# Kernel tuning notes

Measured on AMD Instinct MI355X. Metric: run time of the kernel, lower is better.

## Reference

```python
import jax, jax.numpy as jnp
import numpy as np

HEADS = 16  # init_kwargs['heads']


def setup_inputs() -> dict:
    key = jax.random.key(0)
    k1, k2, k3, k4, k5, k6 = jax.random.split(key, 6)
    N, L, E = 2, 2048, 1024
    return {
        "values": jax.random.normal(k1, (N, L, E), dtype=jnp.float32),
        "key": jax.random.normal(k2, (N, L, E), dtype=jnp.float32),
        "query": jax.random.normal(k3, (N, L, E), dtype=jnp.float32),
        "mask": jax.random.randint(k4, (N, 1, L, L), 0, 2, dtype=jnp.int32),
        # fc_out: Linear(heads*head_dim=E, E) with bias
        "W_out": jax.random.normal(k5, (E, E), dtype=jnp.float32) / np.sqrt(E),
        "b_out": jax.random.normal(k6, (E,), dtype=jnp.float32) * 0.01,
    }


def reference(values, key, query, mask, W_out, b_out):
    N, Lq, E = query.shape
    Lk = key.shape[1]
    H = HEADS
    D = E // H  # head_dim = 64
    q = query.reshape(N, Lq, H, D)
    k = key.reshape(N, Lk, H, D)
    v = values.reshape(N, Lk, H, D)
    # energy: (N, H, Q, K)
    energy = jnp.einsum("nqhd,nkhd->nhqk", q, k)
    # masked_fill BEFORE scaling, as in the original
    energy = jnp.where(mask == 0, jnp.float32(-1e20), energy)
    attn = jax.nn.softmax(energy / np.float32(np.sqrt(D)), axis=3)
    out = jnp.einsum("nhqk,nkhd->nqhd", attn, v).reshape(N, Lq, H * D)
    return out @ W_out.T + b_out
```

## Files before the change

### kernel.cpp

```cpp
#include <hip/hip_runtime.h>

#define L_SEQ  2048
#define EMB    1024
#define NHEAD  16
#define HDIM   64
#define NBATCH 2
#define NT     (L_SEQ / 64)

typedef unsigned short u16;
typedef unsigned int   u32;
typedef unsigned long long u64;
typedef short bf16x8 __attribute__((ext_vector_type(8)));
typedef float f32x4  __attribute__((ext_vector_type(4)));
typedef int   i32x4  __attribute__((ext_vector_type(4)));

static __device__ __forceinline__ u16 f2bf(float x) {
    union { float f; unsigned u; } a; a.f = x;
    unsigned r = a.u + 0x7FFFu + ((a.u >> 16) & 1u);
    return (u16)(r >> 16);
}
static __device__ __forceinline__ void cvt8(const float4& a, const float4& b, u16* o, float s) {
    o[0]=f2bf(a.x*s); o[1]=f2bf(a.y*s); o[2]=f2bf(a.z*s); o[3]=f2bf(a.w*s);
    o[4]=f2bf(b.x*s); o[5]=f2bf(b.y*s); o[6]=f2bf(b.z*s); o[7]=f2bf(b.w*s);
}

static __device__ __forceinline__ u32 cvt_pk_bf16(float lo, float hi) {
    u32 r;
    asm("v_cvt_pk_bf16_f32 %0, %1, %2" : "=v"(r) : "v"(lo), "v"(hi));
    return r;
}
static __device__ __forceinline__ void permswap32(u32 &x, u32 &y) {
    asm("v_permlane32_swap_b32 %0, %1" : "+v"(x), "+v"(y));
}
static __device__ __forceinline__ void permswap16(u32 &x, u32 &y) {
    asm("v_permlane16_swap_b32 %0, %1" : "+v"(x), "+v"(y));
}

static __device__ __forceinline__ void lds_barrier() {
    asm volatile("s_waitcnt lgkmcnt(0)" ::: "memory");
    __builtin_amdgcn_s_barrier();
    __builtin_amdgcn_sched_barrier(0);
}

__global__ __launch_bounds__(256)
void prep_fused(const float* __restrict__ Kg, const float* __restrict__ Vg,
                const int* __restrict__ Mg,
                u16* __restrict__ Kb, u16* __restrict__ Vt,
                u64* __restrict__ maskp)
{
    const int bid = blockIdx.x;
    const int tid = threadIdx.x;
    __shared__ u16 Vl2[64][72];

    if (bid < 1024) {
        const int wave = tid >> 6;
        const int lane = tid & 63;
        const int row  = bid * 4 + wave;
        const int* mp = Mg + (size_t)row * L_SEQ + lane;
        u64* op = maskp + (size_t)row * NT;
        for (int tt = 0; tt < NT; ++tt) {
            u64 b = __ballot(mp[tt * 64] != 0);
            if (lane == 0) op[tt] = b;
        }
    } else {
        const int b  = bid - 1024;
        const int tt = b & 31, hh = (b >> 5) & 15, nn = b >> 9;
        const int row = tid >> 2;
        const int dc  = (tid & 3) * 16;

        const size_t gin = ((size_t)(nn * L_SEQ) + tt * 64 + row) * EMB + hh * HDIM + dc;

        {
            u16 o[16];
            cvt8(*(const float4*)(Kg + gin),     *(const float4*)(Kg + gin + 4),  o,     1.f);
            cvt8(*(const float4*)(Kg + gin + 8), *(const float4*)(Kg + gin + 12), o + 8, 1.f);
            size_t ko = ((size_t)(nn * NHEAD + hh) * L_SEQ + tt * 64 + row) * HDIM + dc;
            *(uint4*)(Kb + ko)     = *(const uint4*)o;
            *(uint4*)(Kb + ko + 8) = *(const uint4*)&o[8];
        }
        {
            u16 o[16];
            cvt8(*(const float4*)(Vg + gin),     *(const float4*)(Vg + gin + 4),  o,     1.f);
            cvt8(*(const float4*)(Vg + gin + 8), *(const float4*)(Vg + gin + 12), o + 8, 1.f);
            #pragma unroll
            for (int j = 0; j < 16; ++j) Vl2[dc + j][row] = o[j];
        }
        __syncthreads();
        {
            const int d  = tid >> 2;
            const int kc = (tid & 3) * 16;
            size_t vo = ((size_t)(nn * NHEAD + hh) * HDIM + d) * L_SEQ + tt * 64 + kc;
            *(uint4*)(Vt + vo)     = *(const uint4*)&Vl2[d][kc];
            *(uint4*)(Vt + vo + 8) = *(const uint4*)&Vl2[d][kc + 8];
        }
    }
}

static __device__ __forceinline__ void pv_step(
    const u32 (&Dwp)[2][8], const u16 (&Vb)[64][72],
    f32x4 (&acc)[2][4], int l16, int quad)
{
    __builtin_amdgcn_s_setprio(1);
    #pragma unroll
    for (int kc = 0; kc < 2; ++kc) {
        bf16x8 pf[2];
        #pragma unroll
        for (int qs = 0; qs < 2; ++qs) {
            u32 b0 = Dwp[qs][4 * kc + 0], b2 = Dwp[qs][4 * kc + 2];
            permswap32(b0, b2); permswap16(b0, b2);
            u32 b1 = Dwp[qs][4 * kc + 1], b3 = Dwp[qs][4 * kc + 3];
            permswap32(b1, b3); permswap16(b1, b3);
            union { i32x4 i; bf16x8 v; } pu;
            pu.i[0] = (int)b0; pu.i[1] = (int)b1; pu.i[2] = (int)b2; pu.i[3] = (int)b3;
            pf[qs] = pu.v;
        }
        #pragma unroll
        for (int dc = 0; dc < 4; ++dc) {
            bf16x8 vf = *(const bf16x8*)&Vb[dc * 16 + l16][kc * 32 + quad * 8];
            acc[0][dc] = __builtin_amdgcn_mfma_f32_16x16x32_bf16(vf, pf[0], acc[0][dc], 0, 0, 0);
            acc[1][dc] = __builtin_amdgcn_mfma_f32_16x16x32_bf16(vf, pf[1], acc[1][dc], 0, 0, 0);
        }
    }
    __builtin_amdgcn_s_setprio(0);
}

static __device__ __forceinline__ void attn_tile(
    int t, int kbuf, int vprev, int kw, int vw,
    u32 (&Dwc)[2][8], u32 (&Dwp)[2][8],
    u16 (&Kl)[2][64][72], u16 (&Vl)[4][64][72],
    const bf16x8 (&qf)[2][2], f32x4 (&acc)[2][4], float (&ls)[2][4],
    uint4& kr0, uint4& kr1, uint4& vr0, uint4& vr1,
    u64& mr0, u64& mr1,
    const u16* kbase, const u16* vbase, const u64* mbase, int mqs,
    int srow, int scol, int l16, int quad)
{
    if (t < NT - 1) {
        *(uint4*)&Kl[kw][srow][scol]     = kr0;
        *(uint4*)&Kl[kw][srow][scol + 8] = kr1;
        *(uint4*)&Vl[vw][srow][scol]     = vr0;
        *(uint4*)&Vl[vw][srow][scol + 8] = vr1;
    }
    u64 mcur0 = mr0, mcur1 = mr1;
    if (t < NT - 1) { mr0 = mbase[t + 1]; mr1 = mbase[mqs + t + 1]; }
    if (t < NT - 2) {
        const u16* kp = kbase + (size_t)((t + 2) * 64 + srow) * HDIM + scol;
        const u16* vp = vbase + (size_t)srow * L_SEQ + (t + 2) * 64 + scol;
        kr0 = *(const uint4*)kp;  kr1 = *(const uint4*)(kp + 8);
        vr0 = *(const uint4*)vp;  vr1 = *(const uint4*)(vp + 8);
    }

    const int sh = quad * 4;
    u32 mlo0 = (u32)mcur0 >> sh, mhi0 = (u32)(mcur0 >> 32) >> sh;
    u32 mlo1 = (u32)mcur1 >> sh, mhi1 = (u32)(mcur1 >> 32) >> sh;
    #pragma unroll
    for (int cc = 0; cc < 4; ++cc) {
        bf16x8 k0 = *(const bf16x8*)&Kl[kbuf][cc * 16 + l16][quad * 8];
        bf16x8 k1 = *(const bf16x8*)&Kl[kbuf][cc * 16 + l16][32 + quad * 8];
        f32x4 z0; z0[0]=0.f; z0[1]=0.f; z0[2]=0.f; z0[3]=0.f;
        f32x4 z1 = z0;
        z0 = __builtin_amdgcn_mfma_f32_16x16x32_bf16(k0, qf[0][0], z0, 0, 0, 0);
        z0 = __builtin_amdgcn_mfma_f32_16x16x32_bf16(k1, qf[0][1], z0, 0, 0, 0);
        z1 = __builtin_amdgcn_mfma_f32_16x16x32_bf16(k0, qf[1][0], z1, 0, 0, 0);
        z1 = __builtin_amdgcn_mfma_f32_16x16x32_bf16(k1, qf[1][1], z1, 0, 0, 0);

        #pragma unroll
        for (int qs = 0; qs < 2; ++qs) {
            const f32x4& z = (qs == 0) ? z0 : z1;
            u32 w = (cc < 2) ? ((qs == 0) ? mlo0 : mlo1)
                             : ((qs == 0) ? mhi0 : mhi1);
            float pv[4];
            #pragma unroll
            for (int r = 0; r < 4; ++r) {
                const int pos = (cc & 1) * 16 + r;
                int sm = (int)(w << (31 - pos)) >> 31;
                float p = __builtin_amdgcn_exp2f(z[r]);
                p = __int_as_float(__float_as_int(p) & sm);
                ls[qs][r] += p;
                pv[r] = p;
            }
            Dwc[qs][2 * cc]     = cvt_pk_bf16(pv[0], pv[1]);
            Dwc[qs][2 * cc + 1] = cvt_pk_bf16(pv[2], pv[3]);
        }
    }

    pv_step(Dwp, Vl[vprev], acc, l16, quad);

    lds_barrier();
}

__global__ __launch_bounds__(256, 2)
void attn_kernel(const float* __restrict__ Qg, const u16* __restrict__ Kb,
                 const u16* __restrict__ Vt, const u64* __restrict__ maskp,
                 u16* __restrict__ Og)
{
    const int i    = blockIdx.x;
    const int x    = i & 7;
    const int s    = i >> 3;
    const int g    = ((s >> 4) << 3) + x;
    const int qblk = s & 15;
    const int h    = g & 15;
    const int n    = g >> 4;

    const int tid  = threadIdx.x;
    const int wave = tid >> 6;
    const int lane = tid & 63;
    const int l16  = lane & 15;
    const int quad = lane >> 4;

    __shared__ u16 Kl[2][64][72];
    __shared__ u16 Vl[4][64][72];

    const int q0 = qblk * 128 + wave * 32;

    bf16x8 qf[2][2];
    {
        const float qscale = 0.125f * 1.44269504f;
        #pragma unroll
        for (int qs = 0; qs < 2; ++qs) {
            const float* qp = Qg + ((size_t)(n * L_SEQ) + q0 + qs * 16 + l16) * EMB + h * HDIM;
            #pragma unroll
            for (int half = 0; half < 2; ++half) {
                float4 a = *(const float4*)(qp + half * 32 + quad * 8);
                float4 b = *(const float4*)(qp + half * 32 + quad * 8 + 4);
                u16 o[8];
                cvt8(a, b, o, qscale);
                qf[qs][half] = *(const bf16x8*)o;
            }
        }
    }

    f32x4 acc[2][4];
    #pragma unroll
    for (int qs = 0; qs < 2; ++qs)
        #pragma unroll
        for (int c = 0; c < 4; ++c)
            #pragma unroll
            for (int r = 0; r < 4; ++r) acc[qs][c][r] = 0.f;
    float ls[2][4];
    #pragma unroll
    for (int qs = 0; qs < 2; ++qs)
        #pragma unroll
        for (int r = 0; r < 4; ++r) ls[qs][r] = 0.f;

    u32 DwA[2][8], DwB[2][8];
    #pragma unroll
    for (int qs = 0; qs < 2; ++qs)
        #pragma unroll
        for (int ii = 0; ii < 8; ++ii) { DwA[qs][ii] = 0u; DwB[qs][ii] = 0u; }

    const u16* kbase = Kb + (size_t)(n * NHEAD + h) * L_SEQ * HDIM;
    const u16* vbase = Vt + (size_t)(n * NHEAD + h) * HDIM * L_SEQ;
    const u64* mbase = maskp + ((size_t)(n * L_SEQ) + q0 + l16) * NT;
    const int  mqs   = 16 * NT;

    const int srow = tid >> 2;
    const int scol = (tid & 3) * 16;

    uint4 kr0, kr1, vr0, vr1;
    u64 mr0, mr1;

    {
        const u16* kp = kbase + (size_t)srow * HDIM + scol;
        const u16* vp = vbase + (size_t)srow * L_SEQ + scol;
        kr0 = *(const uint4*)kp;  kr1 = *(const uint4*)(kp + 8);
        vr0 = *(const uint4*)vp;  vr1 = *(const uint4*)(vp + 8);
    }
    *(uint4*)&Kl[0][srow][scol]     = kr0;
    *(uint4*)&Kl[0][srow][scol + 8] = kr1;
    *(uint4*)&Vl[0][srow][scol]     = vr0;
    *(uint4*)&Vl[0][srow][scol + 8] = vr1;
    {
        u32* vz = (u32*)&Vl[3][0][0];
        #pragma unroll
        for (int ii = 0; ii < 9; ++ii) vz[tid + ii * 256] = 0u;
    }
    {
        const u16* kp = kbase + (size_t)(64 + srow) * HDIM + scol;
        const u16* vp = vbase + (size_t)srow * L_SEQ + 64 + scol;
        kr0 = *(const uint4*)kp;  kr1 = *(const uint4*)(kp + 8);
        vr0 = *(const uint4*)vp;  vr1 = *(const uint4*)(vp + 8);
    }
    mr0 = mbase[0];
    mr1 = mbase[mqs];
    __syncthreads();

    for (int j = 0; j < 8; ++j) {
        const int t = j * 4;
        attn_tile(t + 0, 0, 3, 1, 1, DwA, DwB, Kl, Vl, qf, acc, ls,
                  kr0, kr1, vr0, vr1, mr0, mr1, kbase, vbase, mbase, mqs,
                  srow, scol, l16, quad);
        attn_tile(t + 1, 1, 0, 0, 2, DwB, DwA, Kl, Vl, qf, acc, ls,
                  kr0, kr1, vr0, vr1, mr0, mr1, kbase, vbase, mbase, mqs,
                  srow, scol, l16, quad);
        attn_tile(t + 2, 0, 1, 1, 3, DwA, DwB, Kl, Vl, qf, acc, ls,
                  kr0, kr1, vr0, vr1, mr0, mr1, kbase, vbase, mbase, mqs,
                  srow, scol, l16, quad);
        attn_tile(t + 3, 1, 2, 0, 0, DwB, DwA, Kl, Vl, qf, acc, ls,
                  kr0, kr1, vr0, vr1, mr0, mr1, kbase, vbase, mbase, mqs,
                  srow, scol, l16, quad);
    }

    pv_step(DwB, Vl[3], acc, l16, quad);

    #pragma unroll
    for (int qs = 0; qs < 2; ++qs) {
        float sm = (ls[qs][0] + ls[qs][1]) + (ls[qs][2] + ls[qs][3]);
        sm += __shfl_xor(sm, 16);
        sm += __shfl_xor(sm, 32);
        float inv = 1.f / sm;

        u16* op = Og + ((size_t)(n * L_SEQ) + q0 + qs * 16 + l16) * EMB + h * HDIM + quad * 4;
        #pragma unroll
        for (int dc = 0; dc < 4; ++dc) {
            u32 u0 = cvt_pk_bf16(acc[qs][dc][0] * inv, acc[qs][dc][1] * inv);
            u32 u1 = cvt_pk_bf16(acc[qs][dc][2] * inv, acc[qs][dc][3] * inv);
            uint2 st; st.x = u0; st.y = u1;
            *(uint2*)(op + dc * 16) = st;
        }
    }
}

__global__ __launch_bounds__(512)
void out_gemm(const u16* __restrict__ A, const float* __restrict__ W,
              const float* __restrict__ bias, float* __restrict__ out)
{
    const int i  = blockIdx.x;
    const int bn = i & 7;
    const int bm = i >> 3;

    const int tid = threadIdx.x;
    const int wave = tid >> 6;
    const int lane = tid & 63;
    const int l16  = lane & 15;
    const int quad = lane >> 4;
    const int wr = wave >> 2;
    const int wc = wave & 3;

    __shared__ u16 Al[2][128][72];
    __shared__ u16 Bl[2][128][72];

    f32x4 acc[4][2];
    #pragma unroll
    for (int ii = 0; ii < 4; ++ii)
        #pragma unroll
        for (int j = 0; j < 2; ++j)
            #pragma unroll
            for (int r = 0; r < 4; ++r) acc[ii][j][r] = 0.f;

    const int srow = tid >> 2;
    const int kc   = (tid & 3) * 16;

    const u16*  ap = A + (size_t)(bm * 128 + srow) * EMB + kc;
    const float* bp = W + (size_t)(bn * 128 + srow) * EMB + kc;

    uint4  ar0 = *(const uint4*)ap,      ar1 = *(const uint4*)(ap + 8);
    float4 br0 = *(const float4*)bp,     br1 = *(const float4*)(bp + 4);
    float4 br2 = *(const float4*)(bp + 8), br3 = *(const float4*)(bp + 12);

    #pragma unroll 4
    for (int s = 0; s < 16; ++s) {
        const int b = s & 1;
        *(uint4*)&Al[b][srow][kc]     = ar0;
        *(uint4*)&Al[b][srow][kc + 8] = ar1;
        {
            u16 ob[16];
            cvt8(br0, br1, ob,     1.f);
            cvt8(br2, br3, ob + 8, 1.f);
            *(uint4*)&Bl[b][srow][kc]     = *(const uint4*)ob;
            *(uint4*)&Bl[b][srow][kc + 8] = *(const uint4*)&ob[8];
        }
        if (s < 15) {
            const int k0 = (s + 1) * 64;
            ar0 = *(const uint4*)(ap + k0);       ar1 = *(const uint4*)(ap + k0 + 8);
            br0 = *(const float4*)(bp + k0);      br1 = *(const float4*)(bp + k0 + 4);
            br2 = *(const float4*)(bp + k0 + 8);  br3 = *(const float4*)(bp + k0 + 12);
        }
        lds_barrier();

        #pragma unroll
        for (int kk = 0; kk < 2; ++kk) {
            bf16x8 af[4], bfr[2];
            #pragma unroll
            for (int ii = 0; ii < 4; ++ii)
                af[ii] = *(const bf16x8*)&Al[b][wr * 64 + ii * 16 + l16][kk * 32 + quad * 8];
            #pragma unroll
            for (int j = 0; j < 2; ++j)
                bfr[j] = *(const bf16x8*)&Bl[b][wc * 32 + j * 16 + l16][kk * 32 + quad * 8];
            #pragma unroll
            for (int ii = 0; ii < 4; ++ii)
                #pragma unroll
                for (int j = 0; j < 2; ++j)
                    acc[ii][j] = __builtin_amdgcn_mfma_f32_16x16x32_bf16(af[ii], bfr[j], acc[ii][j], 0, 0, 0);
        }
    }

    #pragma unroll
    for (int j = 0; j < 2; ++j) {
        int col = bn * 128 + wc * 32 + j * 16 + l16;
        float bv = bias[col];
        #pragma unroll
        for (int ii = 0; ii < 4; ++ii) {
            int row0 = bm * 128 + wr * 64 + ii * 16 + quad * 4;
            #pragma unroll
            for (int r = 0; r < 4; ++r)
                out[(size_t)(row0 + r) * EMB + col] = acc[ii][j][r] + bv;
        }
    }
}

extern "C" void kernel_launch(void* const* d_in, const int* in_sizes, int n_in,
                              void* d_out, int out_size, void* d_ws, size_t ws_size,
                              hipStream_t stream)
{
    const float* Vg = (const float*)d_in[0];
    const float* Kg = (const float*)d_in[1];
    const float* Qg = (const float*)d_in[2];
    const int*   Mg = (const int*)d_in[3];
    const float* Wg = (const float*)d_in[4];
    const float* Bg = (const float*)d_in[5];
    float* Og = (float*)d_out;

    const size_t QKV = (size_t)NBATCH * L_SEQ * EMB;
    char* ws = (char*)d_ws;
    u16* attn_ws = (u16*)ws;
    u16* Kb      = (u16*)(ws + QKV * 2);
    u16* Vt      = Kb + QKV;
    u64* maskp   = (u64*)(Vt + QKV);

    prep_fused<<<dim3(2048), 256, 0, stream>>>(Kg, Vg, Mg, Kb, Vt, maskp);

    attn_kernel<<<dim3(512), 256, 0, stream>>>(Qg, Kb, Vt, maskp, attn_ws);

    out_gemm<<<dim3(256), 512, 0, stream>>>(attn_ws, Wg, Bg, Og);
}
```

Baseline: 207.8 us.

## Load V fragments directly from global into registers, bypassing LDS staging

V tiles are no longer staged through a 4-deep LDS ring. Each wave now loads its own bf16x8 V fragments straight from the transposed global V buffer into register double-buffers (VA/VB), one tile ahead of the PV MFMA step. This removes the LDS writes and reads for V and frees shared memory. In exchange, every wave re-fetches the same V tile from global/L2 (4x redundant traffic per block) with only one tile of latency hiding, and register pressure rises by 16 bf16x8 vectors.

```diff
diff --git a/kernel.cpp b/kernel.cpp
--- a/kernel.cpp
+++ b/kernel.cpp
@@ -97,8 +97,8 @@
 }
 
 static __device__ __forceinline__ void pv_step(
-    const u32 (&Dwp)[2][8], const u16 (&Vb)[64][72],
-    f32x4 (&acc)[2][4], int l16, int quad)
+    const u32 (&Dwp)[2][8], const bf16x8 (&vf)[8],
+    f32x4 (&acc)[2][4])
 {
     __builtin_amdgcn_s_setprio(1);
     #pragma unroll
@@ -116,20 +116,20 @@
         }
         #pragma unroll
         for (int dc = 0; dc < 4; ++dc) {
-            bf16x8 vf = *(const bf16x8*)&Vb[dc * 16 + l16][kc * 32 + quad * 8];
-            acc[0][dc] = __builtin_amdgcn_mfma_f32_16x16x32_bf16(vf, pf[0], acc[0][dc], 0, 0, 0);
-            acc[1][dc] = __builtin_amdgcn_mfma_f32_16x16x32_bf16(vf, pf[1], acc[1][dc], 0, 0, 0);
+            acc[0][dc] = __builtin_amdgcn_mfma_f32_16x16x32_bf16(vf[kc * 4 + dc], pf[0], acc[0][dc], 0, 0, 0);
+            acc[1][dc] = __builtin_amdgcn_mfma_f32_16x16x32_bf16(vf[kc * 4 + dc], pf[1], acc[1][dc], 0, 0, 0);
         }
     }
     __builtin_amdgcn_s_setprio(0);
 }
 
 static __device__ __forceinline__ void attn_tile(
-    int t, int kbuf, int vprev, int kw, int vw,
+    int t, int kbuf, int kw,
     u32 (&Dwc)[2][8], u32 (&Dwp)[2][8],
-    u16 (&Kl)[2][64][72], u16 (&Vl)[4][64][72],
+    bf16x8 (&Vcur)[8], const bf16x8 (&Vprev)[8],
+    u16 (&Kl)[2][64][72],
     const bf16x8 (&qf)[2][2], f32x4 (&acc)[2][4], float (&ls)[2][4],
-    uint4& kr0, uint4& kr1, uint4& vr0, uint4& vr1,
+    uint4& kr0, uint4& kr1,
     u64& mr0, u64& mr1,
     const u16* kbase, const u16* vbase, const u64* mbase, int mqs,
     int srow, int scol, int l16, int quad)
@@ -137,16 +137,20 @@
     if (t < NT - 1) {
         *(uint4*)&Kl[kw][srow][scol]     = kr0;
         *(uint4*)&Kl[kw][srow][scol + 8] = kr1;
-        *(uint4*)&Vl[vw][srow][scol]     = vr0;
-        *(uint4*)&Vl[vw][srow][scol + 8] = vr1;
     }
     u64 mcur0 = mr0, mcur1 = mr1;
     if (t < NT - 1) { mr0 = mbase[t + 1]; mr1 = mbase[mqs + t + 1]; }
     if (t < NT - 2) {
         const u16* kp = kbase + (size_t)((t + 2) * 64 + srow) * HDIM + scol;
-        const u16* vp = vbase + (size_t)srow * L_SEQ + (t + 2) * 64 + scol;
         kr0 = *(const uint4*)kp;  kr1 = *(const uint4*)(kp + 8);
-        vr0 = *(const uint4*)vp;  vr1 = *(const uint4*)(vp + 8);
+    }
+    {
+        const u16* vp0 = vbase + (size_t)l16 * L_SEQ + t * 64 + quad * 8;
+        #pragma unroll
+        for (int kc = 0; kc < 2; ++kc)
+            #pragma unroll
+            for (int dc = 0; dc < 4; ++dc)
+                Vcur[kc * 4 + dc] = *(const bf16x8*)(vp0 + (size_t)(dc * 16) * L_SEQ + kc * 32);
     }
 
     const int sh = quad * 4;
@@ -183,7 +187,7 @@
         }
     }
 
-    pv_step(Dwp, Vl[vprev], acc, l16, quad);
+    pv_step(Dwp, Vprev, acc);
 
     lds_barrier();
 }
@@ -208,7 +212,6 @@
     const int quad = lane >> 4;
 
     __shared__ u16 Kl[2][64][72];
-    __shared__ u16 Vl[4][64][72];
 
     const int q0 = qblk * 128 + wave * 32;
 
@@ -248,6 +251,10 @@
         #pragma unroll
         for (int ii = 0; ii < 8; ++ii) { DwA[qs][ii] = 0u; DwB[qs][ii] = 0u; }
 
+    bf16x8 VA[8], VB[8];
+    #pragma unroll
+    for (int ii = 0; ii < 8; ++ii) VB[ii] = (bf16x8)(short)0;
+
     const u16* kbase = Kb + (size_t)(n * NHEAD + h) * L_SEQ * HDIM;
     const u16* vbase = Vt + (size_t)(n * NHEAD + h) * HDIM * L_SEQ;
     const u64* mbase = maskp + ((size_t)(n * L_SEQ) + q0 + l16) * NT;
@@ -256,29 +263,18 @@
     const int srow = tid >> 2;
     const int scol = (tid & 3) * 16;
 
-    uint4 kr0, kr1, vr0, vr1;
+    uint4 kr0, kr1;
     u64 mr0, mr1;
 
     {
         const u16* kp = kbase + (size_t)srow * HDIM + scol;
-        const u16* vp = vbase + (size_t)srow * L_SEQ + scol;
         kr0 = *(const uint4*)kp;  kr1 = *(const uint4*)(kp + 8);
-        vr0 = *(const uint4*)vp;  vr1 = *(const uint4*)(vp + 8);
     }
     *(uint4*)&Kl[0][srow][scol]     = kr0;
     *(uint4*)&Kl[0][srow][scol + 8] = kr1;
-    *(uint4*)&Vl[0][srow][scol]     = vr0;
-    *(uint4*)&Vl[0][srow][scol + 8] = vr1;
-    {
-        u32* vz = (u32*)&Vl[3][0][0];
-        #pragma unroll
-        for (int ii = 0; ii < 9; ++ii) vz[tid + ii * 256] = 0u;
-    }
     {
         const u16* kp = kbase + (size_t)(64 + srow) * HDIM + scol;
-        const u16* vp = vbase + (size_t)srow * L_SEQ + 64 + scol;
         kr0 = *(const uint4*)kp;  kr1 = *(const uint4*)(kp + 8);
-        vr0 = *(const uint4*)vp;  vr1 = *(const uint4*)(vp + 8);
     }
     mr0 = mbase[0];
     mr1 = mbase[mqs];
@@ -286,21 +282,21 @@
 
     for (int j = 0; j < 8; ++j) {
         const int t = j * 4;
-        attn_tile(t + 0, 0, 3, 1, 1, DwA, DwB, Kl, Vl, qf, acc, ls,
-                  kr0, kr1, vr0, vr1, mr0, mr1, kbase, vbase, mbase, mqs,
+        attn_tile(t + 0, 0, 1, DwA, DwB, VA, VB, Kl, qf, acc, ls,
+                  kr0, kr1, mr0, mr1, kbase, vbase, mbase, mqs,
                   srow, scol, l16, quad);
-        attn_tile(t + 1, 1, 0, 0, 2, DwB, DwA, Kl, Vl, qf, acc, ls,
-                  kr0, kr1, vr0, vr1, mr0, mr1, kbase, vbase, mbase, mqs,
+        attn_tile(t + 1, 1, 0, DwB, DwA, VB, VA, Kl, qf, acc, ls,
+                  kr0, kr1, mr0, mr1, kbase, vbase, mbase, mqs,
                   srow, scol, l16, quad);
-        attn_tile(t + 2, 0, 1, 1, 3, DwA, DwB, Kl, Vl, qf, acc, ls,
-                  kr0, kr1, vr0, vr1, mr0, mr1, kbase, vbase, mbase, mqs,
+        attn_tile(t + 2, 0, 1, DwA, DwB, VA, VB, Kl, qf, acc, ls,
+                  kr0, kr1, mr0, mr1, kbase, vbase, mbase, mqs,
                   srow, scol, l16, quad);
-        attn_tile(t + 3, 1, 2, 0, 0, DwB, DwA, Kl, Vl, qf, acc, ls,
-                  kr0, kr1, vr0, vr1, mr0, mr1, kbase, vbase, mbase, mqs,
+        attn_tile(t + 3, 1, 0, DwB, DwA, VB, VA, Kl, qf, acc, ls,
+                  kr0, kr1, mr0, mr1, kbase, vbase, mbase, mqs,
                   srow, scol, l16, quad);
     }
 
-    pv_step(DwB, Vl[3], acc, l16, quad);
+    pv_step(DwB, VB, acc);
 
     #pragma unroll
     for (int qs = 0; qs < 2; ++qs) {
```

Result: slower. 275.3 us (+32.5%).
